# Performance work log

Measured on AMD Instinct MI355X. Metric: run time of the kernel, lower is better.

Reference implementation:

```python
import jax, jax.numpy as jnp
import numpy as np

EPS = 1e-8  # torch.nn.CosineSimilarity default eps
SCALE_WEIGHT = (1.0, 2.0, 3.0, 4.0)  # weight[idx] for 4 scales


def _nearest_labels(lab, H, W):
    # torch F.interpolate mode='nearest': src_idx = floor(dst_idx * in/out)
    H0, W0 = lab.shape[2], lab.shape[3]
    ri = (jnp.arange(H) * H0) // H
    ci = (jnp.arange(W) * W0) // W
    return lab[:, :, ri][:, :, :, ci]


def _scale_loss(pseudo_labels, feat, feat_old, num_class, num_old_class):
    B, C, H, W = feat.shape
    lab = _nearest_labels(pseudo_labels, H, W).reshape(-1)          # [B*H*W]
    f = jnp.transpose(feat, (0, 2, 3, 1)).reshape(-1, C)            # (b h w) c
    fo = jnp.transpose(feat_old, (0, 2, 3, 1)).reshape(-1, C)
    nf = jnp.maximum(jnp.sqrt(jnp.sum(f * f, axis=1)), EPS)
    nfo = jnp.maximum(jnp.sqrt(jnp.sum(fo * fo, axis=1)), EPS)
    sim = jnp.sum(f * fo, axis=1) / (nf * nfo)                      # per-pixel cosine
    # segment-reduce by class; label 255 (ignore) is out-of-range and dropped
    seg = jax.ops.segment_sum(sim, lab, num_segments=num_class)
    cnt = jax.ops.segment_sum(jnp.ones_like(sim), lab, num_segments=num_class)
    mean_sim = seg / jnp.maximum(cnt, 1.0)
    cls = jnp.arange(num_class)
    factor = jnp.where(cls == 0, num_old_class / num_class,
                       jnp.where(cls <= num_old_class, 1.0, 0.0))
    present = cnt > 0
    dis = 1.0 - mean_sim
    return jnp.sum(jnp.where(present, factor * dis, 0.0))


def setup_inputs() -> dict:
    key = jax.random.key(0)
    ks = jax.random.split(key, 9)
    B, C = 8, 256
    sizes = [(128, 128), (64, 64), (32, 32), (16, 16)]
    inp = {
        "pseudo_labels": jax.random.randint(ks[0], (B, 1, 512, 512), 0, 21, dtype=jnp.int64)
        if jax.config.jax_enable_x64 else
        jax.random.randint(ks[0], (B, 1, 512, 512), 0, 21).astype(jnp.int32),
    }
    for i, (h, w) in enumerate(sizes):
        inp[f"f{i}"] = jax.random.normal(ks[1 + i], (B, C, h, w), dtype=jnp.float32)
        inp[f"fo{i}"] = jax.random.normal(ks[5 + i], (B, C, h, w), dtype=jnp.float32)
    inp["num_class"] = 21
    inp["num_old_class"] = 15
    return inp


def reference(pseudo_labels, f0, f1, f2, f3, fo0, fo1, fo2, fo3, num_class, num_old_class):
    feats = (f0, f1, f2, f3)
    feats_old = (fo0, fo1, fo2, fo3)
    loss = jnp.float32(0.0)
    for idx in range(4):
        loss = loss + SCALE_WEIGHT[idx] * _scale_loss(
            pseudo_labels, feats[idx], feats_old[idx], num_class, num_old_class)
    return loss
```

## Files before the change

### kernel.cpp

```cpp
#include <hip/hip_runtime.h>
#include <math.h>


#define EPSV 1e-8f

__global__ __launch_bounds__(512)
void msrd_main(const float* __restrict__ f0, const float* __restrict__ fo0,
               const float* __restrict__ f1, const float* __restrict__ fo1,
               const float* __restrict__ f2, const float* __restrict__ fo2,
               const float* __restrict__ f3, const float* __restrict__ fo3,
               const int*   __restrict__ labels,
               const int*   __restrict__ p_nclass,
               float* __restrict__ ws)
{
    int bid = blockIdx.x;
    int scale, lb, logW, logHW, sshift;
    const float *f, *fo;
    if (bid < 1024)      { scale = 0; lb = bid;        f = f0; fo = fo0; logW = 7; logHW = 14; sshift = 2; }
    else if (bid < 1280) { scale = 1; lb = bid - 1024; f = f1; fo = fo1; logW = 6; logHW = 12; sshift = 3; }
    else if (bid < 1344) { scale = 2; lb = bid - 1280; f = f2; fo = fo2; logW = 5; logHW = 10; sshift = 4; }
    else                 { scale = 3; lb = bid - 1344; f = f3; fo = fo3; logW = 4; logHW = 8;  sshift = 5; }
    const int HW = 1 << logHW;
    const int W  = 1 << logW;

    const int tid  = threadIdx.x;
    const int wave = tid >> 6;
    const int lane = tid & 63;
    const int half = lane >> 5;
    const int gi   = lane & 31;

    const int g   = lb * 32 + gi;
    const int pix = g << 2;
    const int b   = pix >> logHW;
    const int rem = pix & (HW - 1);

    const int c0 = wave * 32 + half * 16;
    const float* __restrict__ fpb  = f  + (((size_t)(b * 256 + c0)) << logHW) + rem;
    const float* __restrict__ fopb = fo + (((size_t)(b * 256 + c0)) << logHW) + rem;

    float dx=0.f,dy=0.f,dz=0.f,dw=0.f;
    float ax=0.f,ay=0.f,az=0.f,aw=0.f;
    float bx=0.f,by=0.f,bz=0.f,bw=0.f;

    #pragma unroll
    for (int batch = 0; batch < 2; ++batch) {
        float4 X[8], Y[8];
        const size_t cb = (size_t)(batch * 8) << logHW;
        #pragma unroll
        for (int j = 0; j < 8; ++j)
            X[j] = *(const float4*)(fpb + cb + ((size_t)j << logHW));
        #pragma unroll
        for (int j = 0; j < 8; ++j)
            Y[j] = *(const float4*)(fopb + cb + ((size_t)j << logHW));
        #pragma unroll
        for (int j = 0; j < 8; ++j) {
            float4 x = X[j], y = Y[j];
            dx = fmaf(x.x, y.x, dx); dy = fmaf(x.y, y.y, dy);
            dz = fmaf(x.z, y.z, dz); dw = fmaf(x.w, y.w, dw);
            ax = fmaf(x.x, x.x, ax); ay = fmaf(x.y, x.y, ay);
            az = fmaf(x.z, x.z, az); aw = fmaf(x.w, x.w, aw);
            bx = fmaf(y.x, y.x, bx); by = fmaf(y.y, y.y, by);
            bz = fmaf(y.z, y.z, bz); bw = fmaf(y.w, y.w, bw);
        }
    }

    dx += __shfl_xor(dx, 32); dy += __shfl_xor(dy, 32);
    dz += __shfl_xor(dz, 32); dw += __shfl_xor(dw, 32);
    ax += __shfl_xor(ax, 32); ay += __shfl_xor(ay, 32);
    az += __shfl_xor(az, 32); aw += __shfl_xor(aw, 32);
    bx += __shfl_xor(bx, 32); by += __shfl_xor(by, 32);
    bz += __shfl_xor(bz, 32); bw += __shfl_xor(bw, 32);

    __shared__ float4 sD[8][32], sA[8][32], sB[8][32];
    __shared__ float bin_sim[32], bin_cnt[32];
    if (tid < 32) { bin_sim[tid] = 0.f; bin_cnt[tid] = 0.f; }
    if (half == 0) {
        sD[wave][gi] = make_float4(dx,dy,dz,dw);
        sA[wave][gi] = make_float4(ax,ay,az,aw);
        sB[wave][gi] = make_float4(bx,by,bz,bw);
    }
    __syncthreads();

    if (tid < 32) {
        float4 D = sD[0][gi], A = sA[0][gi], Bv = sB[0][gi];
        #pragma unroll
        for (int w = 1; w < 8; ++w) {
            float4 t;
            t = sD[w][gi]; D.x += t.x; D.y += t.y; D.z += t.z; D.w += t.w;
            t = sA[w][gi]; A.x += t.x; A.y += t.y; A.z += t.z; A.w += t.w;
            t = sB[w][gi]; Bv.x += t.x; Bv.y += t.y; Bv.z += t.z; Bv.w += t.w;
        }
        const int nclass  = *p_nclass;
        const int labbase = b << 18;
        float Dv[4] = {D.x, D.y, D.z, D.w};
        float Av[4] = {A.x, A.y, A.z, A.w};
        float Bw[4] = {Bv.x, Bv.y, Bv.z, Bv.w};
        #pragma unroll
        for (int j = 0; j < 4; ++j) {
            float na  = fmaxf(sqrtf(Av[j]), EPSV);
            float nb  = fmaxf(sqrtf(Bw[j]), EPSV);
            float sim = Dv[j] / (na * nb);
            int p    = rem + j;
            int h    = p >> logW;
            int col  = p & (W - 1);
            int lidx = labbase + ((h << sshift) << 9) + (col << sshift);
            int lab  = labels[lidx];
            if ((unsigned)lab < (unsigned)nclass) {
                atomicAdd(&bin_sim[lab], sim);
                atomicAdd(&bin_cnt[lab], 1.0f);
            }
        }
    }
    __syncthreads();

    if (tid < 32) {
        float s = bin_sim[tid], c = bin_cnt[tid];
        if (s != 0.f || c != 0.f) {
            atomicAdd(&ws[scale * 64 + tid],      s);
            atomicAdd(&ws[scale * 64 + 32 + tid], c);
        }
    }
}

__global__ void msrd_final(const float* __restrict__ ws,
                           const int* __restrict__ p_nclass,
                           const int* __restrict__ p_nold,
                           float* __restrict__ out)
{
    if (threadIdx.x == 0 && blockIdx.x == 0) {
        const int nc = *p_nclass;
        const int no = *p_nold;
        const float wgt[4] = {1.f, 2.f, 3.f, 4.f};
        float loss = 0.f;
        for (int s = 0; s < 4; ++s) {
            float sl = 0.f;
            for (int c = 0; c < nc && c < 32; ++c) {
                float seg = ws[s * 64 + c];
                float cnt = ws[s * 64 + 32 + c];
                if (cnt > 0.f) {
                    float factor = (c == 0) ? (float)no / (float)nc
                                            : (c <= no ? 1.f : 0.f);
                    sl += factor * (1.f - seg / fmaxf(cnt, 1.f));
                }
            }
            loss += wgt[s] * sl;
        }
        out[0] = loss;
    }
}

extern "C" void kernel_launch(void* const* d_in, const int* in_sizes, int n_in,
                              void* d_out, int out_size, void* d_ws, size_t ws_size,
                              hipStream_t stream) {
    const int*   labels = (const int*)  d_in[0];
    const float* f0  = (const float*)d_in[1];
    const float* fo0 = (const float*)d_in[2];
    const float* f1  = (const float*)d_in[3];
    const float* fo1 = (const float*)d_in[4];
    const float* f2  = (const float*)d_in[5];
    const float* fo2 = (const float*)d_in[6];
    const float* f3  = (const float*)d_in[7];
    const float* fo3 = (const float*)d_in[8];
    const int* p_nclass = (const int*)d_in[9];
    const int* p_nold   = (const int*)d_in[10];
    float* out = (float*)d_out;
    float* ws  = (float*)d_ws;

    hipMemsetAsync(ws, 0, 4 * 64 * sizeof(float), stream);
    msrd_main<<<dim3(1360), dim3(512), 0, stream>>>(f0, fo0, f1, fo1, f2, fo2, f3, fo3,
                                                    labels, p_nclass, ws);
    msrd_final<<<dim3(1), dim3(64), 0, stream>>>(ws, p_nclass, p_nold, out);
}
```

Baseline: 361.8 us.

## Widen per-block pixel tile to 256 and stream channels in groups of four

Each block now covers 256 pixels, with every lane of a wave handling four pixels. Each wave walks its 32 channels in groups of four loads per tensor, with a scheduling barrier between the loads and the FMAs. This drops the half-wave channel split and its shuffle reduction and halves the grid to 680 blocks. Each load instruction now covers 1 KB of contiguous memory per wave, and label atomics are issued once per block for twice as many pixels. The cost is less memory-level parallelism per thread (8 loads in flight instead of 16) and fewer blocks to hide latency.

```diff
diff --git a/kernel.cpp b/kernel.cpp
--- a/kernel.cpp
+++ b/kernel.cpp
@@ -3,6 +3,15 @@
 
 
 #define EPSV 1e-8f
+#define SBAR() __builtin_amdgcn_sched_barrier(0)
+
+#define FMA1(Xv,Yv)                                                          \
+    dx = fmaf(Xv.x, Yv.x, dx); dy = fmaf(Xv.y, Yv.y, dy);                    \
+    dz = fmaf(Xv.z, Yv.z, dz); dw = fmaf(Xv.w, Yv.w, dw);                    \
+    ax = fmaf(Xv.x, Xv.x, ax); ay = fmaf(Xv.y, Xv.y, ay);                    \
+    az = fmaf(Xv.z, Xv.z, az); aw = fmaf(Xv.w, Xv.w, aw);                    \
+    bx = fmaf(Yv.x, Yv.x, bx); by = fmaf(Yv.y, Yv.y, by);                    \
+    bz = fmaf(Yv.z, Yv.z, bz); bw = fmaf(Yv.w, Yv.w, bw);
 
 __global__ __launch_bounds__(512)
 void msrd_main(const float* __restrict__ f0, const float* __restrict__ fo0,
@@ -13,85 +22,69 @@
                const int*   __restrict__ p_nclass,
                float* __restrict__ ws)
 {
-    int bid = blockIdx.x;
+    const int bid = blockIdx.x;
     int scale, lb, logW, logHW, sshift;
     const float *f, *fo;
-    if (bid < 1024)      { scale = 0; lb = bid;        f = f0; fo = fo0; logW = 7; logHW = 14; sshift = 2; }
-    else if (bid < 1280) { scale = 1; lb = bid - 1024; f = f1; fo = fo1; logW = 6; logHW = 12; sshift = 3; }
-    else if (bid < 1344) { scale = 2; lb = bid - 1280; f = f2; fo = fo2; logW = 5; logHW = 10; sshift = 4; }
-    else                 { scale = 3; lb = bid - 1344; f = f3; fo = fo3; logW = 4; logHW = 8;  sshift = 5; }
-    const int HW = 1 << logHW;
-    const int W  = 1 << logW;
+    if (bid < 512)      { scale = 0; lb = bid;       f = f0; fo = fo0; logW = 7; logHW = 14; sshift = 2; }
+    else if (bid < 640) { scale = 1; lb = bid - 512; f = f1; fo = fo1; logW = 6; logHW = 12; sshift = 3; }
+    else if (bid < 672) { scale = 2; lb = bid - 640; f = f2; fo = fo2; logW = 5; logHW = 10; sshift = 4; }
+    else                { scale = 3; lb = bid - 672; f = f3; fo = fo3; logW = 4; logHW = 8;  sshift = 5; }
+    const int W = 1 << logW;
 
     const int tid  = threadIdx.x;
     const int wave = tid >> 6;
     const int lane = tid & 63;
-    const int half = lane >> 5;
-    const int gi   = lane & 31;
 
-    const int g   = lb * 32 + gi;
-    const int pix = g << 2;
-    const int b   = pix >> logHW;
-    const int rem = pix & (HW - 1);
+    const int lbpi = logHW - 8;
+    const int img  = lb >> lbpi;
+    const int po   = (lb - (img << lbpi)) << 8;
+    const int rem  = po + (lane << 2);
 
-    const int c0 = wave * 32 + half * 16;
-    const float* __restrict__ fpb  = f  + (((size_t)(b * 256 + c0)) << logHW) + rem;
-    const float* __restrict__ fopb = fo + (((size_t)(b * 256 + c0)) << logHW) + rem;
+    const int c0 = wave << 5;
+    const float* __restrict__ fp  = f  + (((size_t)(img * 256 + c0)) << logHW) + rem;
+    const float* __restrict__ fop = fo + (((size_t)(img * 256 + c0)) << logHW) + rem;
+    const size_t cs = (size_t)1 << logHW;
 
     float dx=0.f,dy=0.f,dz=0.f,dw=0.f;
     float ax=0.f,ay=0.f,az=0.f,aw=0.f;
     float bx=0.f,by=0.f,bz=0.f,bw=0.f;
 
     #pragma unroll
-    for (int batch = 0; batch < 2; ++batch) {
-        float4 X[8], Y[8];
-        const size_t cb = (size_t)(batch * 8) << logHW;
-        #pragma unroll
-        for (int j = 0; j < 8; ++j)
-            X[j] = *(const float4*)(fpb + cb + ((size_t)j << logHW));
-        #pragma unroll
-        for (int j = 0; j < 8; ++j)
-            Y[j] = *(const float4*)(fopb + cb + ((size_t)j << logHW));
-        #pragma unroll
-        for (int j = 0; j < 8; ++j) {
-            float4 x = X[j], y = Y[j];
-            dx = fmaf(x.x, y.x, dx); dy = fmaf(x.y, y.y, dy);
-            dz = fmaf(x.z, y.z, dz); dw = fmaf(x.w, y.w, dw);
-            ax = fmaf(x.x, x.x, ax); ay = fmaf(x.y, x.y, ay);
-            az = fmaf(x.z, x.z, az); aw = fmaf(x.w, x.w, aw);
-            bx = fmaf(y.x, y.x, bx); by = fmaf(y.y, y.y, by);
-            bz = fmaf(y.z, y.z, bz); bw = fmaf(y.w, y.w, bw);
-        }
+    for (int cc = 0; cc < 32; cc += 4) {
+        const float* pf = fp  + (size_t)cc * cs;
+        const float* pq = fop + (size_t)cc * cs;
+        float4 X0, X1, X2, X3, Y0, Y1, Y2, Y3;
+        X0 = *(const float4*)(pf);
+        X1 = *(const float4*)(pf + cs);
+        X2 = *(const float4*)(pf + 2*cs);
+        X3 = *(const float4*)(pf + 3*cs);
+        Y0 = *(const float4*)(pq);
+        Y1 = *(const float4*)(pq + cs);
+        Y2 = *(const float4*)(pq + 2*cs);
+        Y3 = *(const float4*)(pq + 3*cs);
+        SBAR();
+        FMA1(X0, Y0) FMA1(X1, Y1) FMA1(X2, Y2) FMA1(X3, Y3)
     }
 
-    dx += __shfl_xor(dx, 32); dy += __shfl_xor(dy, 32);
-    dz += __shfl_xor(dz, 32); dw += __shfl_xor(dw, 32);
-    ax += __shfl_xor(ax, 32); ay += __shfl_xor(ay, 32);
-    az += __shfl_xor(az, 32); aw += __shfl_xor(aw, 32);
-    bx += __shfl_xor(bx, 32); by += __shfl_xor(by, 32);
-    bz += __shfl_xor(bz, 32); bw += __shfl_xor(bw, 32);
-
-    __shared__ float4 sD[8][32], sA[8][32], sB[8][32];
+    __shared__ float4 sD[8][64], sA[8][64], sB[8][64];
     __shared__ float bin_sim[32], bin_cnt[32];
     if (tid < 32) { bin_sim[tid] = 0.f; bin_cnt[tid] = 0.f; }
-    if (half == 0) {
-        sD[wave][gi] = make_float4(dx,dy,dz,dw);
-        sA[wave][gi] = make_float4(ax,ay,az,aw);
-        sB[wave][gi] = make_float4(bx,by,bz,bw);
-    }
+    sD[wave][lane] = make_float4(dx,dy,dz,dw);
+    sA[wave][lane] = make_float4(ax,ay,az,aw);
+    sB[wave][lane] = make_float4(bx,by,bz,bw);
     __syncthreads();
 
-    if (tid < 32) {
-        float4 D = sD[0][gi], A = sA[0][gi], Bv = sB[0][gi];
+    if (tid < 64) {
+        float4 D = sD[0][lane], A = sA[0][lane], Bv = sB[0][lane];
         #pragma unroll
         for (int w = 1; w < 8; ++w) {
             float4 t;
-            t = sD[w][gi]; D.x += t.x; D.y += t.y; D.z += t.z; D.w += t.w;
-            t = sA[w][gi]; A.x += t.x; A.y += t.y; A.z += t.z; A.w += t.w;
-            t = sB[w][gi]; Bv.x += t.x; Bv.y += t.y; Bv.z += t.z; Bv.w += t.w;
+            t = sD[w][lane]; D.x += t.x; D.y += t.y; D.z += t.z; D.w += t.w;
+            t = sA[w][lane]; A.x += t.x; A.y += t.y; A.z += t.z; A.w += t.w;
+            t = sB[w][lane]; Bv.x += t.x; Bv.y += t.y; Bv.z += t.z; Bv.w += t.w;
         }
         const int nclass  = *p_nclass;
-        const int labbase = b << 18;
+        const int labbase = img << 18;
         float Dv[4] = {D.x, D.y, D.z, D.w};
         float Av[4] = {A.x, A.y, A.z, A.w};
         float Bw[4] = {Bv.x, Bv.y, Bv.z, Bv.w};
@@ -167,7 +160,7 @@
     float* ws  = (float*)d_ws;
 
     hipMemsetAsync(ws, 0, 4 * 64 * sizeof(float), stream);
-    msrd_main<<<dim3(1360), dim3(512), 0, stream>>>(f0, fo0, f1, fo1, f2, fo2, f3, fo3,
-                                                    labels, p_nclass, ws);
+    msrd_main<<<dim3(680), dim3(512), 0, stream>>>(f0, fo0, f1, fo1, f2, fo2, f3, fo3,
+                                                   labels, p_nclass, ws);
     msrd_final<<<dim3(1), dim3(64), 0, stream>>>(ws, p_nclass, p_nold, out);
 }
```

New measurement: 360.2 us. Within noise of the previous version (-0.4%).
